# Optimization experiments

Hardware: AMD Instinct MI355X
Metric: run time of the kernel (lower is better)

Reference implementation:

```python
import jax, jax.numpy as jnp
import numpy as np

B, H, W, DIM, R = 8, 64, 64, 768, 16
_DN = ('NHWC', 'HWIO', 'NHWC')


def _conv(x, k):
    # stride-1 SAME conv == torch Conv2d(padding=k//2) for 3x3 and 1x1 kernels
    return jax.lax.conv_general_dilated(x, k, (1, 1), 'SAME', dimension_numbers=_DN)


def setup_inputs() -> dict:
    key = jax.random.key(0)
    ks = jax.random.split(key, 16)
    s = 0.02
    return {
        'x': jax.random.normal(ks[0], (B, H, W, DIM), jnp.float32),
        'W_qkv': jax.random.normal(ks[1], (DIM, 3 * DIM), jnp.float32) * s,
        'b_qkv': jax.random.normal(ks[2], (3 * DIM,), jnp.float32) * s,
        'Wa_q': jax.random.normal(ks[3], (DIM, R), jnp.float32) * s,
        'Wb_q': jax.random.normal(ks[4], (R, DIM), jnp.float32) * s,
        'Wa_v': jax.random.normal(ks[5], (DIM, R), jnp.float32) * s,
        'Wb_v': jax.random.normal(ks[6], (R, DIM), jnp.float32) * s,
        'K_q3': jax.random.normal(ks[7], (3, 3, R, R), jnp.float32) * s,
        'b_q3': jax.random.normal(ks[8], (R,), jnp.float32) * s,
        'K_v3': jax.random.normal(ks[9], (3, 3, R, R), jnp.float32) * s,
        'b_v3': jax.random.normal(ks[10], (R,), jnp.float32) * s,
        'K_q1': jax.random.normal(ks[11], (1, 1, R, R), jnp.float32) * s,
        'b_q1': jax.random.normal(ks[12], (R,), jnp.float32) * s,
        'K_v1': jax.random.normal(ks[13], (1, 1, R, R), jnp.float32) * s,
        'b_v1': jax.random.normal(ks[14], (R,), jnp.float32) * s,
    }


def reference(x, W_qkv, b_qkv, Wa_q, Wb_q, Wa_v, Wb_v,
              K_q3, b_q3, K_v3, b_v3, K_q1, b_q1, K_v1, b_v1):
    dim = x.shape[-1]
    # base QKV projection: [B,H,W,3*dim]
    qkv = jnp.einsum('bhwc,cd->bhwd', x, W_qkv) + b_qkv
    # low-rank down-projections: [B,H,W,r]
    a_q = x @ Wa_q
    a_v = x @ Wa_v
    # NHWC convs replace the permute->conv->permute dance in the torch code
    mid_q = _conv(a_q, K_q3) + b_q3 + _conv(a_q, K_q1) + b_q1 + a_q
    mid_v = _conv(a_v, K_v3) + b_v3 + _conv(a_v, K_v1) + b_v1 + a_v
    new_q = mid_q @ Wb_q  # [B,H,W,dim]
    new_v = mid_v @ Wb_v
    qkv = qkv.at[..., :dim].add(new_q)
    qkv = qkv.at[..., -dim:].add(new_v)
    return qkv
```

## Files before the change

### kernel.cpp

```cpp
#include <hip/hip_runtime.h>

typedef __bf16 bf16;
typedef __attribute__((ext_vector_type(8))) __bf16 bf16x8;
typedef __attribute__((ext_vector_type(4))) float f32x4;

#define AS1U(p) ((const __attribute__((address_space(1))) unsigned int*)(p))
#define AS3U(p) ((__attribute__((address_space(3))) unsigned int*)(p))

__device__ __forceinline__ unsigned short f2bf(float f) {
    union { float f; unsigned int u; } a; a.f = f;
    unsigned int u = a.u;
    u += 0x7fffu + ((u >> 16) & 1u);
    return (unsigned short)(u >> 16);
}
__device__ __forceinline__ unsigned int pk2(float a, float b) {
    return (unsigned int)f2bf(a) | ((unsigned int)f2bf(b) << 16);
}

#define MTOT 32768
#define DIM  768
#define KP   832
#define NOUT 2304

__global__ __launch_bounds__(256) void bbuild_kernel(
    const float* __restrict__ Wqkv, const float* __restrict__ Wbq,
    const float* __restrict__ Wbv, const float* __restrict__ Waq,
    const float* __restrict__ Wav, unsigned short* __restrict__ Bt,
    unsigned short* __restrict__ WaT)
{
    const int bx = blockIdx.x;
    const int t = threadIdx.x;
    if (bx < 432) {
        __shared__ float Ts[64][65];
        const int kt = bx % 12, nt = bx / 12;
        #pragma unroll
        for (int it = 0; it < 4; ++it) {
            int idx = it * 256 + t;
            int kr = idx >> 4;
            int nc = (idx & 15) * 4;
            float4 v = *(const float4*)(Wqkv + (size_t)(kt * 64 + kr) * NOUT + nt * 64 + nc);
            Ts[kr][nc + 0] = v.x; Ts[kr][nc + 1] = v.y;
            Ts[kr][nc + 2] = v.z; Ts[kr][nc + 3] = v.w;
        }
        __syncthreads();
        #pragma unroll
        for (int it = 0; it < 4; ++it) {
            int idx = it * 256 + t;
            int nr = idx >> 4;
            int kc = (idx & 15) * 4;
            ushort4 u;
            u.x = f2bf(Ts[kc + 0][nr]); u.y = f2bf(Ts[kc + 1][nr]);
            u.z = f2bf(Ts[kc + 2][nr]); u.w = f2bf(Ts[kc + 3][nr]);
            *(ushort4*)(Bt + (size_t)(nt * 64 + nr) * KP + kt * 64 + kc) = u;
        }
    } else if (bx < 576) {
        int idx = (bx - 432) * 256 + t;
        int n = idx >> 4;
        int k = 768 + (idx & 15) * 4;
        ushort4 u;
        unsigned short* up = (unsigned short*)&u;
        #pragma unroll
        for (int j = 0; j < 4; ++j) {
            int kk = k + j;
            float v = 0.f;
            if (kk < 784) { if (n < 768) v = Wbq[(size_t)(kk - 768) * 768 + n]; }
            else if (kk < 800) { if (n >= 1536) v = Wbv[(size_t)(kk - 784) * 768 + (n - 1536)]; }
            up[j] = f2bf(v);
        }
        *(ushort4*)(Bt + (size_t)n * KP + k) = u;
    } else {
        int idx = (bx - 576) * 256 + t;
        int n = idx / 768, k = idx % 768;
        float v = (n < 16) ? Waq[(size_t)k * 16 + n] : Wav[(size_t)k * 16 + (n - 16)];
        WaT[(size_t)n * 768 + k] = f2bf(v);
    }
}

__global__ __launch_bounds__(256) void prep_kernel(
    const float* __restrict__ x, const bf16* __restrict__ WaT,
    unsigned short* __restrict__ Ap, float* __restrict__ aq, float* __restrict__ av)
{
    __shared__ bf16 Xs[64 * 64];
    const int t = threadIdx.x;
    const int wave = t >> 6, lane = t & 63;
    const int l15 = lane & 15, q = lane >> 4;
    const int p0 = blockIdx.x * 64;
    const int row = t >> 2, c16 = (t & 3) * 16;
    const int r8 = row & 7, ch0 = c16 >> 3;
    f32x4 acc[2] = {};

    for (int kt = 0; kt < 12; ++kt) {
        const float* xp = x + (size_t)(p0 + row) * DIM + kt * 64 + c16;
        float4 v0 = *(const float4*)(xp + 0);
        float4 v1 = *(const float4*)(xp + 4);
        float4 v2 = *(const float4*)(xp + 8);
        float4 v3 = *(const float4*)(xp + 12);
        uint4 u0, u1;
        u0.x = pk2(v0.x, v0.y); u0.y = pk2(v0.z, v0.w);
        u0.z = pk2(v1.x, v1.y); u0.w = pk2(v1.z, v1.w);
        u1.x = pk2(v2.x, v2.y); u1.y = pk2(v2.z, v2.w);
        u1.z = pk2(v3.x, v3.y); u1.w = pk2(v3.z, v3.w);
        unsigned short* apq = Ap + (size_t)(p0 + row) * KP + kt * 64 + c16;
        *(uint4*)(apq) = u0;
        *(uint4*)(apq + 8) = u1;
        __syncthreads();
        *(uint4*)(Xs + row * 64 + ((ch0 + 0) ^ r8) * 8) = u0;
        *(uint4*)(Xs + row * 64 + ((ch0 + 1) ^ r8) * 8) = u1;
        __syncthreads();
        bf16x8 bfr[2][2];
        #pragma unroll
        for (int kk = 0; kk < 2; ++kk)
            #pragma unroll
            for (int nf = 0; nf < 2; ++nf)
                bfr[kk][nf] = *(const bf16x8*)(WaT + (size_t)(nf * 16 + l15) * 768
                                               + kt * 64 + kk * 32 + q * 8);
        #pragma unroll
        for (int kk = 0; kk < 2; ++kk) {
            int phys = ((kk << 2) + q) ^ (l15 & 7);
            bf16x8 af = *(const bf16x8*)(Xs + (wave * 16 + l15) * 64 + phys * 8);
            acc[0] = __builtin_amdgcn_mfma_f32_16x16x32_bf16(af, bfr[kk][0], acc[0], 0, 0, 0);
            acc[1] = __builtin_amdgcn_mfma_f32_16x16x32_bf16(af, bfr[kk][1], acc[1], 0, 0, 0);
        }
    }
    const int m = wave * 16 + q * 4;
    #pragma unroll
    for (int r = 0; r < 4; ++r) {
        aq[(size_t)(p0 + m + r) * 16 + l15] = acc[0][r];
        av[(size_t)(p0 + m + r) * 16 + l15] = acc[1][r];
    }
    uint4 z; z.x = z.y = z.z = z.w = 0u;
    *(uint4*)(Ap + (size_t)(p0 + row) * KP + 800 + (t & 3) * 8) = z;
}

__global__ __launch_bounds__(256) void conv_mid_kernel(
    const float* __restrict__ aq, const float* __restrict__ av,
    const float* __restrict__ Kq3, const float* __restrict__ bq3,
    const float* __restrict__ Kv3, const float* __restrict__ bv3,
    const float* __restrict__ Kq1, const float* __restrict__ bq1,
    const float* __restrict__ Kv1, const float* __restrict__ bv1,
    unsigned short* __restrict__ Ap)
{
    const int bx = blockIdx.x;
    const int qv   = bx & 1;
    const int tile = (bx >> 1) & 15;
    const int b    = bx >> 5;
    const float* a  = qv ? av  : aq;
    const float* K3 = qv ? Kv3 : Kq3;
    const float* K1 = qv ? Kv1 : Kq1;
    const float* b3 = qv ? bv3 : bq3;
    const float* b1 = qv ? bv1 : bq1;

    __shared__ float K3s[9][16][16];
    __shared__ float K1s[16][16];
    const int t = threadIdx.x;
    for (int i = t; i < 9 * 256; i += 256) ((float*)K3s)[i] = K3[i];
    ((float*)K1s)[t] = K1[t];
    __syncthreads();

    const int lh = t >> 4, lw = t & 15;
    const int h = (tile >> 2) * 16 + lh;
    const int w = (tile & 3) * 16 + lw;

    float acc[16];
    const float* ac = a + (((size_t)b * 64 + h) * 64 + w) * 16;
    float cen[16];
    #pragma unroll
    for (int i4 = 0; i4 < 4; ++i4) {
        float4 qd = ((const float4*)ac)[i4];
        cen[i4 * 4 + 0] = qd.x; cen[i4 * 4 + 1] = qd.y;
        cen[i4 * 4 + 2] = qd.z; cen[i4 * 4 + 3] = qd.w;
    }
    #pragma unroll
    for (int o = 0; o < 16; ++o) acc[o] = b3[o] + b1[o] + cen[o];
    #pragma unroll
    for (int i = 0; i < 16; ++i) {
        float vi = cen[i];
        #pragma unroll
        for (int o = 0; o < 16; ++o) acc[o] += vi * K1s[i][o];
    }
    for (int dh = -1; dh <= 1; ++dh) {
        for (int dw = -1; dw <= 1; ++dw) {
            int hh = h + dh, ww = w + dw;
            if ((unsigned)hh < 64u && (unsigned)ww < 64u) {
                const float* ap = a + (((size_t)b * 64 + hh) * 64 + ww) * 16;
                float v[16];
                #pragma unroll
                for (int i4 = 0; i4 < 4; ++i4) {
                    float4 qd = ((const float4*)ap)[i4];
                    v[i4 * 4 + 0] = qd.x; v[i4 * 4 + 1] = qd.y;
                    v[i4 * 4 + 2] = qd.z; v[i4 * 4 + 3] = qd.w;
                }
                const int tap = (dh + 1) * 3 + (dw + 1);
                #pragma unroll
                for (int i = 0; i < 16; ++i) {
                    float vi = v[i];
                    #pragma unroll
                    for (int o = 0; o < 16; ++o) acc[o] += vi * K3s[tap][i][o];
                }
            }
        }
    }
    unsigned short* dst = Ap + (((size_t)b * 64 + h) * 64 + w) * KP + 768 + qv * 16;
    #pragma unroll
    for (int o4 = 0; o4 < 4; ++o4) {
        ushort4 u;
        u.x = f2bf(acc[o4 * 4 + 0]); u.y = f2bf(acc[o4 * 4 + 1]);
        u.z = f2bf(acc[o4 * 4 + 2]); u.w = f2bf(acc[o4 * 4 + 3]);
        *(ushort4*)(dst + o4 * 4) = u;
    }
}

__global__ __launch_bounds__(256, 2) void gemm_kernel(
    const bf16* __restrict__ A, const bf16* __restrict__ Bt,
    const float* __restrict__ bias, float* __restrict__ out)
{
    __shared__ bf16 As[128 * 64];
    __shared__ bf16 Bs[128 * 64];
    const int t = threadIdx.x;
    const int wave = t >> 6, lane = t & 63;
    const int m0 = blockIdx.y * 128, n0 = blockIdx.x * 128;
    const int wm = wave & 1, wn = wave >> 1;

    f32x4 acc[4][4] = {};

    const int sr = lane >> 3;
    const int ql = (lane & 7) ^ sr;

    for (int kt = 0; kt < 13; ++kt) {
        const int k0 = kt * 64;
        __syncthreads();
        #pragma unroll
        for (int it = 0; it < 4; ++it) {
            int ci = wave * 4 + it;
            int r = ci * 8 + sr;
            const bf16* ga = A  + (size_t)(m0 + r) * KP + k0 + ql * 8;
            __builtin_amdgcn_global_load_lds(AS1U(ga), AS3U(As + ci * 512 + lane * 8), 16, 0, 0);
            const bf16* gb = Bt + (size_t)(n0 + r) * KP + k0 + ql * 8;
            __builtin_amdgcn_global_load_lds(AS1U(gb), AS3U(Bs + ci * 512 + lane * 8), 16, 0, 0);
        }
        __syncthreads();
        #pragma unroll
        for (int kk = 0; kk < 2; ++kk) {
            bf16x8 af[4], bfr[4];
            const int phys = ((kk << 2) + (lane >> 4)) ^ (lane & 7);
            #pragma unroll
            for (int mi = 0; mi < 4; ++mi) {
                int rr = wm * 64 + mi * 16 + (lane & 15);
                af[mi] = *(const bf16x8*)(As + rr * 64 + phys * 8);
            }
            #pragma unroll
            for (int ni = 0; ni < 4; ++ni) {
                int rr = wn * 64 + ni * 16 + (lane & 15);
                bfr[ni] = *(const bf16x8*)(Bs + rr * 64 + phys * 8);
            }
            #pragma unroll
            for (int mi = 0; mi < 4; ++mi)
                #pragma unroll
                for (int ni = 0; ni < 4; ++ni)
                    acc[mi][ni] = __builtin_amdgcn_mfma_f32_16x16x32_bf16(
                        af[mi], bfr[ni], acc[mi][ni], 0, 0, 0);
        }
    }
    #pragma unroll
    for (int ni = 0; ni < 4; ++ni) {
        int col = n0 + wn * 64 + ni * 16 + (lane & 15);
        float bv = bias[col];
        #pragma unroll
        for (int mi = 0; mi < 4; ++mi) {
            int rbase = m0 + wm * 64 + mi * 16 + ((lane >> 4) << 2);
            #pragma unroll
            for (int r = 0; r < 4; ++r)
                out[(size_t)(rbase + r) * NOUT + col] = acc[mi][ni][r] + bv;
        }
    }
}

extern "C" void kernel_launch(void* const* d_in, const int* in_sizes, int n_in,
                              void* d_out, int out_size, void* d_ws, size_t ws_size,
                              hipStream_t stream) {
    const float* x    = (const float*)d_in[0];
    const float* Wqkv = (const float*)d_in[1];
    const float* bqkv = (const float*)d_in[2];
    const float* Waq  = (const float*)d_in[3];
    const float* Wbq  = (const float*)d_in[4];
    const float* Wav  = (const float*)d_in[5];
    const float* Wbv  = (const float*)d_in[6];
    const float* Kq3  = (const float*)d_in[7];
    const float* bq3  = (const float*)d_in[8];
    const float* Kv3  = (const float*)d_in[9];
    const float* bv3  = (const float*)d_in[10];
    const float* Kq1  = (const float*)d_in[11];
    const float* bq1  = (const float*)d_in[12];
    const float* Kv1  = (const float*)d_in[13];
    const float* bv1  = (const float*)d_in[14];
    float* out = (float*)d_out;

    char* ws = (char*)d_ws;
    unsigned short* Ap  = (unsigned short*)ws;
    float* aq           = (float*)(ws + 54525952);
    float* av           = (float*)(ws + 54525952 + 2097152);
    unsigned short* Bt  = (unsigned short*)(ws + 54525952 + 4194304);
    unsigned short* WaT = (unsigned short*)(ws + 62554112);

    bbuild_kernel<<<672, 256, 0, stream>>>(Wqkv, Wbq, Wbv, Waq, Wav, Bt, WaT);
    prep_kernel<<<MTOT / 64, 256, 0, stream>>>(x, (const bf16*)WaT, Ap, aq, av);
    conv_mid_kernel<<<256, 256, 0, stream>>>(aq, av, Kq3, bq3, Kv3, bv3,
                                             Kq1, bq1, Kv1, bv1, Ap);
    gemm_kernel<<<dim3(NOUT / 128, MTOT / 128), 256, 0, stream>>>(
        (const bf16*)Ap, (const bf16*)Bt, bqkv, out);
}
```

Measured before the change: 562.3 us.

## Enlarge GEMM tile to 256x256 with double-buffered LDS and interleaved MFMA phases

The main GEMM moves from 128x128 tiles with 4 waves to 256x256 tiles with 8 waves, each wave computing a 128x64 sub-tile. LDS is double-buffered so the next K-slab is issued with global_load_lds before computing the current one, and explicit vmcnt waits replace the two __syncthreads per iteration. The MFMA work is split into four phases separated by barriers and raised wave priority. Together these aim to raise arithmetic intensity and overlap loads with math, at the cost of 128KB of LDS per block, more accumulator registers, and fewer blocks in the grid.

```diff
diff --git a/kernel.cpp b/kernel.cpp
--- a/kernel.cpp
+++ b/kernel.cpp
@@ -210,64 +210,100 @@
     }
 }
 
-__global__ __launch_bounds__(256, 2) void gemm_kernel(
+__global__ __launch_bounds__(512, 2) void gemm_kernel(
     const bf16* __restrict__ A, const bf16* __restrict__ Bt,
     const float* __restrict__ bias, float* __restrict__ out)
 {
-    __shared__ bf16 As[128 * 64];
-    __shared__ bf16 Bs[128 * 64];
+    __shared__ bf16 As[2][256 * 64];
+    __shared__ bf16 Bs[2][256 * 64];
     const int t = threadIdx.x;
     const int wave = t >> 6, lane = t & 63;
-    const int m0 = blockIdx.y * 128, n0 = blockIdx.x * 128;
-    const int wm = wave & 1, wn = wave >> 1;
-
-    f32x4 acc[4][4] = {};
-
-    const int sr = lane >> 3;
-    const int ql = (lane & 7) ^ sr;
+    const int wm = wave >> 2, wn = wave & 3;
+    const int m0 = blockIdx.y * 256, n0 = blockIdx.x * 256;
+
+    const int sr8 = lane >> 3;
+    const int slc = (lane & 7) ^ sr8;
+    const bf16* gA = A  + (size_t)(m0 + wave * 8 + sr8) * KP + slc * 8;
+    const bf16* gB = Bt + (size_t)(n0 + wave * 8 + sr8) * KP + slc * 8;
+    const int ldsbase = wave * 512 + lane * 8;
+
+    const int l15 = lane & 15;
+    const int q   = lane >> 4;
+    const int l7  = lane & 7;
+
+    f32x4 acc[8][4] = {};
+
+    auto STAGE = [&](int kt1, int bufi) {
+        const int k0 = kt1 * 64;
+        #pragma unroll
+        for (int it = 0; it < 4; ++it) {
+            __builtin_amdgcn_global_load_lds(AS1U(gA + (size_t)(it * 64) * KP + k0),
+                AS3U(&As[bufi][it * 4096 + ldsbase]), 16, 0, 0);
+            __builtin_amdgcn_global_load_lds(AS1U(gB + (size_t)(it * 64) * KP + k0),
+                AS3U(&Bs[bufi][it * 4096 + ldsbase]), 16, 0, 0);
+        }
+    };
+
+    STAGE(0, 0);
 
     for (int kt = 0; kt < 13; ++kt) {
-        const int k0 = kt * 64;
-        __syncthreads();
-        #pragma unroll
-        for (int it = 0; it < 4; ++it) {
-            int ci = wave * 4 + it;
-            int r = ci * 8 + sr;
-            const bf16* ga = A  + (size_t)(m0 + r) * KP + k0 + ql * 8;
-            __builtin_amdgcn_global_load_lds(AS1U(ga), AS3U(As + ci * 512 + lane * 8), 16, 0, 0);
-            const bf16* gb = Bt + (size_t)(n0 + r) * KP + k0 + ql * 8;
-            __builtin_amdgcn_global_load_lds(AS1U(gb), AS3U(Bs + ci * 512 + lane * 8), 16, 0, 0);
-        }
-        __syncthreads();
+        const int cur = kt & 1;
+        __builtin_amdgcn_sched_barrier(0);
+        if (kt < 12) {
+            STAGE(kt + 1, cur ^ 1);
+            asm volatile("s_waitcnt vmcnt(8)" ::: "memory");
+        } else {
+            asm volatile("s_waitcnt vmcnt(0)" ::: "memory");
+        }
+        __builtin_amdgcn_s_barrier();
+
+        const bf16* as = &As[cur][0];
+        const bf16* bs = &Bs[cur][0];
+
+        bf16x8 bfr[2][4];
         #pragma unroll
         for (int kk = 0; kk < 2; ++kk) {
-            bf16x8 af[4], bfr[4];
-            const int phys = ((kk << 2) + (lane >> 4)) ^ (lane & 7);
-            #pragma unroll
-            for (int mi = 0; mi < 4; ++mi) {
-                int rr = wm * 64 + mi * 16 + (lane & 15);
-                af[mi] = *(const bf16x8*)(As + rr * 64 + phys * 8);
+            const int phys = ((kk << 2) + q) ^ l7;
+            #pragma unroll
+            for (int ni = 0; ni < 4; ++ni)
+                bfr[kk][ni] = *(const bf16x8*)(bs + (wn * 64 + ni * 16 + l15) * 64 + phys * 8);
+        }
+
+        #pragma unroll
+        for (int p = 0; p < 4; ++p) {
+            bf16x8 af[2][2];
+            #pragma unroll
+            for (int j = 0; j < 2; ++j) {
+                const int mi = p * 2 + j;
+                #pragma unroll
+                for (int kk = 0; kk < 2; ++kk) {
+                    const int phys = ((kk << 2) + q) ^ l7;
+                    af[j][kk] = *(const bf16x8*)(as + (wm * 128 + mi * 16 + l15) * 64 + phys * 8);
+                }
             }
-            #pragma unroll
-            for (int ni = 0; ni < 4; ++ni) {
-                int rr = wn * 64 + ni * 16 + (lane & 15);
-                bfr[ni] = *(const bf16x8*)(Bs + rr * 64 + phys * 8);
-            }
-            #pragma unroll
-            for (int mi = 0; mi < 4; ++mi)
+            __builtin_amdgcn_s_barrier();
+            asm volatile("s_waitcnt lgkmcnt(0)" ::: "memory");
+            __builtin_amdgcn_s_setprio(1);
+            #pragma unroll
+            for (int j = 0; j < 2; ++j)
                 #pragma unroll
                 for (int ni = 0; ni < 4; ++ni)
-                    acc[mi][ni] = __builtin_amdgcn_mfma_f32_16x16x32_bf16(
-                        af[mi], bfr[ni], acc[mi][ni], 0, 0, 0);
-        }
-    }
+                    #pragma unroll
+                    for (int kk = 0; kk < 2; ++kk)
+                        acc[p * 2 + j][ni] = __builtin_amdgcn_mfma_f32_16x16x32_bf16(
+                            af[j][kk], bfr[kk][ni], acc[p * 2 + j][ni], 0, 0, 0);
+            __builtin_amdgcn_s_setprio(0);
+            __builtin_amdgcn_s_barrier();
+        }
+    }
+
     #pragma unroll
     for (int ni = 0; ni < 4; ++ni) {
-        int col = n0 + wn * 64 + ni * 16 + (lane & 15);
-        float bv = bias[col];
-        #pragma unroll
-        for (int mi = 0; mi < 4; ++mi) {
-            int rbase = m0 + wm * 64 + mi * 16 + ((lane >> 4) << 2);
+        const int col = n0 + wn * 64 + ni * 16 + l15;
+        const float bv = bias[col];
+        #pragma unroll
+        for (int mi = 0; mi < 8; ++mi) {
+            const int rbase = m0 + wm * 128 + mi * 16 + (q << 2);
             #pragma unroll
             for (int r = 0; r < 4; ++r)
                 out[(size_t)(rbase + r) * NOUT + col] = acc[mi][ni][r] + bv;
@@ -306,6 +342,6 @@
     prep_kernel<<<MTOT / 64, 256, 0, stream>>>(x, (const bf16*)WaT, Ap, aq, av);
     conv_mid_kernel<<<256, 256, 0, stream>>>(aq, av, Kq3, bq3, Kv3, bv3,
                                              Kq1, bq1, Kv1, bv1, Ap);
-    gemm_kernel<<<dim3(NOUT / 128, MTOT / 128), 256, 0, stream>>>(
+    gemm_kernel<<<dim3(NOUT / 256, MTOT / 256), 512, 0, stream>>>(
         (const bf16*)Ap, (const bf16*)Bt, bqkv, out);
 }
```

New measurement: 601.9 us. +7.0%, slower.
